# Kernel tuning notes

Measured on AMD Instinct MI355X. Metric: run time of the kernel, lower is better.

The kernel has to match this reference:

```python
import jax, jax.numpy as jnp
import numpy as np

B = 16
N = [20000, 5000, 1250, 313, 79]          # node counts per pooling level (fine -> coarse)
E = [120000, 30000, 7500, 1878, 474]      # ~6 edges per node (triangle mesh)
FILTERS = [3, 32, 32, 64, 64, 64]
K = 6
Z = 64
COND = 2
N_LAYERS = 4


def setup_inputs():
    ks = iter(jax.random.split(jax.random.key(0), 64))
    inp = {}
    inp["x"] = jax.random.normal(next(ks), (B * N[0], FILTERS[0]), jnp.float32)
    inp["label"] = jax.random.normal(next(ks), (B, COND), jnp.float32)
    for i in range(5):
        inp[f"edges{i}"] = jax.random.randint(next(ks), (2, E[i]), 0, N[i])
    for i in range(4):
        inp[f"ds_idx{i}"] = jax.random.randint(next(ks), (N[i + 1],), 0, N[i])
        inp[f"us_idx{i}"] = jax.random.randint(next(ks), (N[i], 3), 0, N[i + 1])
        inp[f"us_w{i}"] = jax.random.uniform(next(ks), (N[i], 3), jnp.float32)
    for i in range(4):
        inp[f"enc_w{i}"] = 0.1 * jax.random.normal(next(ks), (K, FILTERS[i], FILTERS[i + 1]), jnp.float32)
        inp[f"enc_b{i}"] = 0.1 * jax.random.normal(next(ks), (FILTERS[i + 1],), jnp.float32)
    for i in range(5):
        inp[f"dec_w{i}"] = 0.1 * jax.random.normal(next(ks), (K, FILTERS[-i - 1], FILTERS[-i - 2]), jnp.float32)
    for i in range(4):
        inp[f"dec_b{i}"] = 0.1 * jax.random.normal(next(ks), (FILTERS[-i - 2],), jnp.float32)
    lat_in = N[4] * FILTERS[-1]
    inp["enc_mu_w"] = 0.1 * jax.random.normal(next(ks), (lat_in, Z), jnp.float32)
    inp["enc_mu_b"] = jnp.zeros((Z,), jnp.float32)
    inp["enc_lv_w"] = 0.1 * jax.random.normal(next(ks), (lat_in, Z), jnp.float32)
    inp["enc_lv_b"] = jnp.zeros((Z,), jnp.float32)
    inp["dec_lin_w"] = 0.1 * jax.random.normal(next(ks), (Z + COND, lat_in), jnp.float32)
    inp["dec_lin_b"] = jnp.zeros((lat_in,), jnp.float32)
    return inp


def _sym_norm(edges, n):
    # ChebConv_Coma.norm: norm = D^-1/2[row] * w * D^-1/2[col], unit weights
    row, col = edges[0], edges[1]
    deg = jnp.zeros((n,), jnp.float32).at[row].add(1.0)
    dinv = jnp.where(deg > 0, deg ** -0.5, 0.0)
    return dinv[row] * dinv[col]


def _cheb(x, edges, norm, W, b):
    # Chebyshev recursion: Tx_0=x, Tx_1=L~x, Tx_k=2 L~ Tx_{k-1} - Tx_{k-2}
    src, tgt = edges[0], edges[1]

    def prop(h):  # h: [B, Nn, F] -> scatter-sum of norm-weighted source features
        return jnp.zeros_like(h).at[:, tgt].add(h[:, src] * norm[None, :, None])

    Tx0 = x
    out = jnp.einsum('bnf,fg->bng', Tx0, W[0])
    Tx1 = prop(x)
    out = out + jnp.einsum('bnf,fg->bng', Tx1, W[1])
    for k in range(2, W.shape[0]):
        Tx2 = 2.0 * prop(Tx1) - Tx0
        out = out + jnp.einsum('bnf,fg->bng', Tx2, W[k])
        Tx0, Tx1 = Tx1, Tx2
    return out if b is None else out + b


def _forward(x, label, us_ws, enc_ws, enc_bs, dec_ws, dec_bs,
             enc_mu_w, enc_mu_b, enc_lv_w, enc_lv_b, dec_lin_w, dec_lin_b,
             edges, norms, ds_idx, us_idx):
    h = x.reshape(B, N[0], FILTERS[0])
    # encoder
    for i in range(N_LAYERS):
        h = jax.nn.relu(_cheb(h, edges[i], norms[i], enc_ws[i], enc_bs[i]))
        h = h[:, ds_idx[i]]  # binary downsample matrix == row gather
    h = h.reshape(B, N[4] * FILTERS[-1])
    mu = h @ enc_mu_w + enc_mu_b
    logvar = h @ enc_lv_w + enc_lv_b
    # reparameterize (fixed eps for determinism)
    eps = jax.random.normal(jax.random.key(42), mu.shape, mu.dtype)
    z = mu + eps * jnp.exp(0.5 * logvar)
    # decoder
    h = jnp.concatenate([z, label], axis=1)
    h = jax.nn.relu(h @ dec_lin_w + dec_lin_b).reshape(B, N[4], FILTERS[-1])
    for i in range(N_LAYERS):
        lvl = N_LAYERS - 1 - i
        # barycentric upsample: 3 nonzeros per output row
        h = jnp.einsum('rk,brkf->brf', us_ws[lvl], h[:, us_idx[lvl]])
        h = jax.nn.relu(_cheb(h, edges[lvl], norms[lvl], dec_ws[i], dec_bs[i]))
    # faithful quirk of the original: final conv uses A_edge_index[-1] (coarsest graph edges)
    h = _cheb(h, edges[-1], norms[-1], dec_ws[4], None)
    return h.reshape(-1, FILTERS[0]), mu, logvar


def reference(x, label,
              edges0, edges1, edges2, edges3, edges4,
              ds_idx0, ds_idx1, ds_idx2, ds_idx3,
              us_idx0, us_idx1, us_idx2, us_idx3,
              us_w0, us_w1, us_w2, us_w3,
              enc_w0, enc_w1, enc_w2, enc_w3,
              enc_b0, enc_b1, enc_b2, enc_b3,
              dec_w0, dec_w1, dec_w2, dec_w3, dec_w4,
              dec_b0, dec_b1, dec_b2, dec_b3,
              enc_mu_w, enc_mu_b, enc_lv_w, enc_lv_b, dec_lin_w, dec_lin_b):
    edges = [edges0, edges1, edges2, edges3, edges4]
    norms = [_sym_norm(edges[i], N[i]) for i in range(5)]
    return _forward(x, label,
                    [us_w0, us_w1, us_w2, us_w3],
                    [enc_w0, enc_w1, enc_w2, enc_w3],
                    [enc_b0, enc_b1, enc_b2, enc_b3],
                    [dec_w0, dec_w1, dec_w2, dec_w3, dec_w4],
                    [dec_b0, dec_b1, dec_b2, dec_b3],
                    enc_mu_w, enc_mu_b, enc_lv_w, enc_lv_b, dec_lin_w, dec_lin_b,
                    edges, norms,
                    [ds_idx0, ds_idx1, ds_idx2, ds_idx3],
                    [us_idx0, us_idx1, us_idx2, us_idx3])
```

## Files before the change

### kernel.cpp

```cpp
#include <hip/hip_runtime.h>
#include <cstdint>
#include <cstddef>

#define WG 256
#define NB 16



__global__ void k_zero_i(int* __restrict__ p, int n) {
  int i = blockIdx.x * WG + threadIdx.x;
  if (i < n) p[i] = 0;
}

__global__ void k_hist(const int* __restrict__ edges, int E,
                       int* __restrict__ dsrc, int* __restrict__ dtgt) {
  int e = blockIdx.x * WG + threadIdx.x;
  if (e >= E) return;
  atomicAdd(&dsrc[edges[e]], 1);
  atomicAdd(&dtgt[edges[E + e]], 1);
}

__global__ void k_scan(const int* __restrict__ deg, int N,
                       int* __restrict__ rowptr, int* __restrict__ cursor) {
  __shared__ int s[WG];
  int t = threadIdx.x;
  int chunk = (N + WG - 1) / WG;
  int a = t * chunk;
  int b = min(N, a + chunk);
  int sum = 0;
  for (int i = a; i < b; i++) sum += deg[i];
  s[t] = sum;
  __syncthreads();
  for (int off = 1; off < WG; off <<= 1) {
    int v = (t >= off) ? s[t - off] : 0;
    __syncthreads();
    s[t] += v;
    __syncthreads();
  }
  int run = (t == 0) ? 0 : s[t - 1];
  for (int i = a; i < b; i++) {
    rowptr[i] = run;
    cursor[i] = run;
    run += deg[i];
  }
  if (t == 0) rowptr[N] = s[WG - 1];
}

__global__ void k_fill(const int* __restrict__ edges, int E,
                       const int* __restrict__ dsrc, int* __restrict__ cursor,
                       int* __restrict__ csrc, float* __restrict__ csw) {
  int e = blockIdx.x * WG + threadIdx.x;
  if (e >= E) return;
  int s = edges[e], t = edges[E + e];
  float da = (float)dsrc[s], db = (float)dsrc[t];
  float wa = (da > 0.f) ? (1.0f / sqrtf(da)) : 0.f;
  float wb = (db > 0.f) ? (1.0f / sqrtf(db)) : 0.f;
  int pos = atomicAdd(&cursor[t], 1);
  csrc[pos] = s;
  csw[pos] = wa * wb;
}

__global__ void k_tr_x(const float* __restrict__ x, float* __restrict__ out) {
  int i = blockIdx.x * WG + threadIdx.x;
  if (i >= NB * 20000 * 3) return;
  int f = i % 3;
  int b = (i / 3) % NB;
  int n = i / 48;
  out[i] = x[((size_t)b * 20000 + n) * 3 + f];
}


static __device__ __forceinline__ float erfinv_f(float x) {
  float w = -log1pf(-x * x);
  float p;
  if (w < 5.0f) {
    w -= 2.5f;
    p = 2.81022636e-08f;
    p = fmaf(p, w, 3.43273939e-07f);
    p = fmaf(p, w, -3.5233877e-06f);
    p = fmaf(p, w, -4.39150654e-06f);
    p = fmaf(p, w, 0.00021858087f);
    p = fmaf(p, w, -0.00125372503f);
    p = fmaf(p, w, -0.00417768164f);
    p = fmaf(p, w, 0.246640727f);
    p = fmaf(p, w, 1.50140941f);
  } else {
    w = sqrtf(w) - 3.0f;
    p = -0.000200214257f;
    p = fmaf(p, w, 0.000100950558f);
    p = fmaf(p, w, 0.00134934322f);
    p = fmaf(p, w, -0.00367342844f);
    p = fmaf(p, w, 0.00573950773f);
    p = fmaf(p, w, -0.0076224613f);
    p = fmaf(p, w, 0.00943887047f);
    p = fmaf(p, w, 1.00167406f);
    p = fmaf(p, w, 2.83297682f);
  }
  return p * x;
}

static __device__ __forceinline__ float bits_to_normal(unsigned b) {
  float f = __uint_as_float((b >> 9) | 0x3f800000u) - 1.0f;
  const float lo = -0.99999994f;
  float u = f * (1.0f - lo) + lo;
  u = fmaxf(u, lo);
  return 1.41421356f * erfinv_f(u);
}

__global__ void k_eps(float* __restrict__ eps) {
  int i = blockIdx.x * WG + threadIdx.x;
  if (i >= 1024) return;
  unsigned x0 = 0u, x1 = (unsigned)i;
  unsigned ks[3] = {0u, 42u, 0u ^ 42u ^ 0x1BD11BDAu};
  x0 += ks[0];
  x1 += ks[1];
  const int R[2][4] = {{13, 15, 26, 6}, {17, 29, 16, 24}};
#pragma unroll
  for (int it = 0; it < 5; it++) {
#pragma unroll
    for (int j = 0; j < 4; j++) {
      x0 += x1;
      int r = R[it & 1][j];
      x1 = (x1 << r) | (x1 >> (32 - r));
      x1 ^= x0;
    }
    x0 += ks[(it + 1) % 3];
    x1 += ks[(it + 2) % 3] + (unsigned)(it + 1);
  }
  eps[i] = bits_to_normal(x0 ^ x1);
}


template <int F>
__global__ __launch_bounds__(WG) void k_propw(const float* __restrict__ in,
                                              float* __restrict__ out,
                                              const float* __restrict__ sub, float scale,
                                              const int* __restrict__ rowptr,
                                              const int* __restrict__ csrc,
                                              const float* __restrict__ csw, int N) {
  constexpr int C4 = F / 16;
  int node = blockIdx.x * 4 + (threadIdx.x >> 6);
  if (node >= N) return;
  int lane = threadIdx.x & 63;
  const float4* in4 = (const float4*)in;
  float4 acc[C4];
#pragma unroll
  for (int u = 0; u < C4; u++) acc[u] = make_float4(0.f, 0.f, 0.f, 0.f);
  int beg = rowptr[node], end = rowptr[node + 1];
  int j = beg;
  for (; j + 1 < end; j += 2) {
    int s0 = __builtin_amdgcn_readfirstlane(csrc[j]);
    int s1 = __builtin_amdgcn_readfirstlane(csrc[j + 1]);
    float w0 = __int_as_float(__builtin_amdgcn_readfirstlane(__float_as_int(csw[j])));
    float w1 = __int_as_float(__builtin_amdgcn_readfirstlane(__float_as_int(csw[j + 1])));
    const float4* r0 = in4 + (size_t)s0 * (4 * F) + lane;
    const float4* r1 = in4 + (size_t)s1 * (4 * F) + lane;
#pragma unroll
    for (int u = 0; u < C4; u++) {
      float4 v0 = r0[u * 64];
      float4 v1 = r1[u * 64];
      acc[u].x = fmaf(w0, v0.x, acc[u].x); acc[u].y = fmaf(w0, v0.y, acc[u].y);
      acc[u].z = fmaf(w0, v0.z, acc[u].z); acc[u].w = fmaf(w0, v0.w, acc[u].w);
      acc[u].x = fmaf(w1, v1.x, acc[u].x); acc[u].y = fmaf(w1, v1.y, acc[u].y);
      acc[u].z = fmaf(w1, v1.z, acc[u].z); acc[u].w = fmaf(w1, v1.w, acc[u].w);
    }
  }
  if (j < end) {
    int s0 = __builtin_amdgcn_readfirstlane(csrc[j]);
    float w0 = __int_as_float(__builtin_amdgcn_readfirstlane(__float_as_int(csw[j])));
    const float4* r0 = in4 + (size_t)s0 * (4 * F) + lane;
#pragma unroll
    for (int u = 0; u < C4; u++) {
      float4 v0 = r0[u * 64];
      acc[u].x = fmaf(w0, v0.x, acc[u].x); acc[u].y = fmaf(w0, v0.y, acc[u].y);
      acc[u].z = fmaf(w0, v0.z, acc[u].z); acc[u].w = fmaf(w0, v0.w, acc[u].w);
    }
  }
  float4* o4 = (float4*)out + (size_t)node * (4 * F) + lane;
  if (sub) {
    const float4* s4 = (const float4*)sub + (size_t)node * (4 * F) + lane;
#pragma unroll
    for (int u = 0; u < C4; u++) {
      float4 sv = s4[u * 64];
      float4 r;
      r.x = fmaf(scale, acc[u].x, -sv.x); r.y = fmaf(scale, acc[u].y, -sv.y);
      r.z = fmaf(scale, acc[u].z, -sv.z); r.w = fmaf(scale, acc[u].w, -sv.w);
      o4[u * 64] = r;
    }
  } else {
#pragma unroll
    for (int u = 0; u < C4; u++) {
      float4 r;
      r.x = scale * acc[u].x; r.y = scale * acc[u].y;
      r.z = scale * acc[u].z; r.w = scale * acc[u].w;
      o4[u * 64] = r;
    }
  }
}

__global__ __launch_bounds__(WG) void k_propw3(const float* __restrict__ in,
                                               float* __restrict__ out,
                                               const float* __restrict__ sub, float scale,
                                               const int* __restrict__ rowptr,
                                               const int* __restrict__ csrc,
                                               const float* __restrict__ csw, int N) {
  int node = blockIdx.x * 4 + (threadIdx.x >> 6);
  if (node >= N) return;
  int lane = threadIdx.x & 63;
  if (lane >= 48) return;
  float acc = 0.f;
  int beg = rowptr[node], end = rowptr[node + 1];
  for (int j = beg; j < end; j++) {
    int s = __builtin_amdgcn_readfirstlane(csrc[j]);
    float w = __int_as_float(__builtin_amdgcn_readfirstlane(__float_as_int(csw[j])));
    acc = fmaf(w, in[(size_t)s * 48 + lane], acc);
  }
  float r = scale * acc;
  if (sub) r -= sub[(size_t)node * 48 + lane];
  out[(size_t)node * 48 + lane] = r;
}

struct Ptr3 {
  const float* p[3];
};

template <int F, int G>
__global__ __launch_bounds__(WG) void k_gemm3(Ptr3 txs, const float* __restrict__ W,
                                              const float* __restrict__ bias,
                                              float* __restrict__ out, int rows,
                                              int accum, int relu) {
  constexpr int CG = G / 4;
  constexpr int RPB = WG / CG;
  __shared__ float sW[3 * F * G];
  for (int i = threadIdx.x; i < 3 * F * G; i += WG) sW[i] = W[i];
  __syncthreads();
  int cg = threadIdx.x % CG;
  int r = threadIdx.x / CG;
  int row = blockIdx.x * RPB + r;
  if (row >= rows) return;
  float* o = out + (size_t)row * G + cg * 4;
  float4 a;
  if (accum) {
    a = *(const float4*)o;
  } else if (bias) {
    a = *(const float4*)(bias + cg * 4);
  } else {
    a = make_float4(0.f, 0.f, 0.f, 0.f);
  }
#pragma unroll
  for (int kk = 0; kk < 3; kk++) {
    const float* t = txs.p[kk] + (size_t)row * F;
    const float* w = sW + kk * F * G + cg * 4;
    if constexpr (F == 3) {
      float x0 = t[0], x1 = t[1], x2 = t[2];
      float4 w0 = *(const float4*)(w + 0 * G);
      float4 w1 = *(const float4*)(w + 1 * G);
      float4 w2 = *(const float4*)(w + 2 * G);
      a.x = fmaf(x0, w0.x, a.x); a.y = fmaf(x0, w0.y, a.y); a.z = fmaf(x0, w0.z, a.z); a.w = fmaf(x0, w0.w, a.w);
      a.x = fmaf(x1, w1.x, a.x); a.y = fmaf(x1, w1.y, a.y); a.z = fmaf(x1, w1.z, a.z); a.w = fmaf(x1, w1.w, a.w);
      a.x = fmaf(x2, w2.x, a.x); a.y = fmaf(x2, w2.y, a.y); a.z = fmaf(x2, w2.z, a.z); a.w = fmaf(x2, w2.w, a.w);
    } else {
#pragma unroll
      for (int f = 0; f < F; f += 4) {
        float4 xv = *(const float4*)(t + f);
        float4 w0 = *(const float4*)(w + (f + 0) * G);
        float4 w1 = *(const float4*)(w + (f + 1) * G);
        float4 w2 = *(const float4*)(w + (f + 2) * G);
        float4 w3 = *(const float4*)(w + (f + 3) * G);
        a.x = fmaf(xv.x, w0.x, a.x); a.y = fmaf(xv.x, w0.y, a.y); a.z = fmaf(xv.x, w0.z, a.z); a.w = fmaf(xv.x, w0.w, a.w);
        a.x = fmaf(xv.y, w1.x, a.x); a.y = fmaf(xv.y, w1.y, a.y); a.z = fmaf(xv.y, w1.z, a.z); a.w = fmaf(xv.y, w1.w, a.w);
        a.x = fmaf(xv.z, w2.x, a.x); a.y = fmaf(xv.z, w2.y, a.y); a.z = fmaf(xv.z, w2.z, a.z); a.w = fmaf(xv.z, w2.w, a.w);
        a.x = fmaf(xv.w, w3.x, a.x); a.y = fmaf(xv.w, w3.y, a.y); a.z = fmaf(xv.w, w3.z, a.z); a.w = fmaf(xv.w, w3.w, a.w);
      }
    }
  }
  if (relu) {
    a.x = fmaxf(a.x, 0.f); a.y = fmaxf(a.y, 0.f);
    a.z = fmaxf(a.z, 0.f); a.w = fmaxf(a.w, 0.f);
  }
  *(float4*)o = a;
}

__global__ __launch_bounds__(WG) void k_final_short(const float* __restrict__ in,
                                                    const float* __restrict__ W,
                                                    float* __restrict__ out) {
  __shared__ float sW[96];
  if (threadIdx.x < 96)
    sW[threadIdx.x] = W[threadIdx.x] - W[192 + threadIdx.x] + W[384 + threadIdx.x];
  __syncthreads();
  int tid = blockIdx.x * WG + threadIdx.x;
  if (tid >= NB * 20000) return;
  int b = tid / 20000, n = tid % 20000;
  const float* t = in + ((size_t)n * 16 + b) * 32;
  float a0 = 0.f, a1 = 0.f, a2 = 0.f;
#pragma unroll
  for (int f = 0; f < 32; f += 4) {
    float4 v = *(const float4*)(t + f);
    a0 = fmaf(v.x, sW[(f + 0) * 3 + 0], a0); a1 = fmaf(v.x, sW[(f + 0) * 3 + 1], a1); a2 = fmaf(v.x, sW[(f + 0) * 3 + 2], a2);
    a0 = fmaf(v.y, sW[(f + 1) * 3 + 0], a0); a1 = fmaf(v.y, sW[(f + 1) * 3 + 1], a1); a2 = fmaf(v.y, sW[(f + 1) * 3 + 2], a2);
    a0 = fmaf(v.z, sW[(f + 2) * 3 + 0], a0); a1 = fmaf(v.z, sW[(f + 2) * 3 + 1], a1); a2 = fmaf(v.z, sW[(f + 2) * 3 + 2], a2);
    a0 = fmaf(v.w, sW[(f + 3) * 3 + 0], a0); a1 = fmaf(v.w, sW[(f + 3) * 3 + 1], a1); a2 = fmaf(v.w, sW[(f + 3) * 3 + 2], a2);
  }
  float* o = out + (size_t)tid * 3;
  o[0] = a0; o[1] = a1; o[2] = a2;
}

__global__ __launch_bounds__(256) void k_final_fix(const float* __restrict__ in,
                                                   const float* __restrict__ W,
                                                   const int* __restrict__ rowptr,
                                                   const int* __restrict__ csrc,
                                                   const float* __restrict__ csw,
                                                   float* __restrict__ out) {
  __shared__ float B0[79 * 32], B1[79 * 32], B2[79 * 32];
  __shared__ float sacc[79 * 3];
  __shared__ float sW[576];
  int b = blockIdx.x, t = threadIdx.x;
  for (int i = t; i < 576; i += 256) sW[i] = W[i];
  for (int i = t; i < 2528; i += 256) {
    int r = i >> 5, f = i & 31;
    B0[i] = in[((size_t)r * 16 + b) * 32 + f];
  }
  __syncthreads();
  for (int i = t; i < 237; i += 256) {
    int r = i / 3, g = i % 3;
    float a = 0.f;
    for (int f = 0; f < 32; f++) a = fmaf(B0[r * 32 + f], sW[f * 3 + g], a);
    sacc[i] = a;
  }
  for (int i = t; i < 2528; i += 256) {
    int r = i >> 5, f = i & 31;
    float a = 0.f;
    for (int j = rowptr[r]; j < rowptr[r + 1]; j++) a = fmaf(csw[j], B0[csrc[j] * 32 + f], a);
    B1[i] = a;
  }
  __syncthreads();
  for (int i = t; i < 237; i += 256) {
    int r = i / 3, g = i % 3;
    float a = sacc[i];
    for (int f = 0; f < 32; f++) a = fmaf(B1[r * 32 + f], sW[96 + f * 3 + g], a);
    sacc[i] = a;
  }
  for (int i = t; i < 2528; i += 256) {
    int r = i >> 5, f = i & 31;
    float a = 0.f;
    for (int j = rowptr[r]; j < rowptr[r + 1]; j++) a = fmaf(csw[j], B1[csrc[j] * 32 + f], a);
    B2[i] = 2.f * a - B0[i];
  }
  __syncthreads();
  for (int i = t; i < 237; i += 256) {
    int r = i / 3, g = i % 3;
    float a = sacc[i];
    for (int f = 0; f < 32; f++) a = fmaf(B2[r * 32 + f], sW[192 + f * 3 + g], a);
    sacc[i] = a;
  }
  __syncthreads();
  for (int i = t; i < 2528; i += 256) {
    int r = i >> 5, f = i & 31;
    float a = 0.f;
    for (int j = rowptr[r]; j < rowptr[r + 1]; j++) a = fmaf(csw[j], B2[csrc[j] * 32 + f], a);
    B0[i] = 2.f * a - B1[i];
  }
  __syncthreads();
  for (int i = t; i < 237; i += 256) {
    int r = i / 3, g = i % 3;
    float a = sacc[i];
    for (int f = 0; f < 32; f++) a = fmaf(B0[r * 32 + f], sW[288 + f * 3 + g], a);
    sacc[i] = a;
  }
  __syncthreads();
  for (int i = t; i < 2528; i += 256) {
    int r = i >> 5, f = i & 31;
    float a = 0.f;
    for (int j = rowptr[r]; j < rowptr[r + 1]; j++) a = fmaf(csw[j], B0[csrc[j] * 32 + f], a);
    B1[i] = 2.f * a - B2[i];
  }
  __syncthreads();
  for (int i = t; i < 237; i += 256) {
    int r = i / 3, g = i % 3;
    float a = sacc[i];
    for (int f = 0; f < 32; f++) a = fmaf(B1[r * 32 + f], sW[384 + f * 3 + g], a);
    sacc[i] = a;
  }
  __syncthreads();
  for (int i = t; i < 2528; i += 256) {
    int r = i >> 5, f = i & 31;
    float a = 0.f;
    for (int j = rowptr[r]; j < rowptr[r + 1]; j++) a = fmaf(csw[j], B1[csrc[j] * 32 + f], a);
    B2[i] = 2.f * a - B0[i];
  }
  __syncthreads();
  for (int i = t; i < 237; i += 256) {
    int r = i / 3, g = i % 3;
    float a = sacc[i];
    for (int f = 0; f < 32; f++) a = fmaf(B2[r * 32 + f], sW[480 + f * 3 + g], a);
    out[((size_t)b * 20000 + r) * 3 + g] = a;
  }
}

template <int F>
__global__ __launch_bounds__(WG) void k_ds(const float* __restrict__ in,
                                           float* __restrict__ out,
                                           const int* __restrict__ idx, int Nout) {
  int i = blockIdx.x * WG + threadIdx.x;
  int total = Nout * NB * F;
  if (i >= total) return;
  int pos = i % (NB * F);
  int j = i / (NB * F);
  float v = in[(size_t)idx[j] * NB * F + pos];
  out[i] = fmaxf(v, 0.f);
}

template <int F>
__global__ __launch_bounds__(WG) void k_us(const float* __restrict__ in,
                                           float* __restrict__ out,
                                           const int* __restrict__ uidx,
                                           const float* __restrict__ uw, int Nf) {
  int i = blockIdx.x * WG + threadIdx.x;
  int total = Nf * NB * F;
  if (i >= total) return;
  int pos = i % (NB * F);
  int r = i / (NB * F);
  float acc = 0.f;
#pragma unroll
  for (int k = 0; k < 3; k++) {
    float v = in[(size_t)uidx[r * 3 + k] * NB * F + pos];
    acc = fmaf(uw[r * 3 + k], fmaxf(v, 0.f), acc);
  }
  out[i] = acc;
}


__global__ __launch_bounds__(64) void k_latent(const float* __restrict__ h,
                                               const float* __restrict__ muW,
                                               const float* __restrict__ muB,
                                               const float* __restrict__ lvW,
                                               const float* __restrict__ lvB,
                                               const float* __restrict__ eps,
                                               const float* __restrict__ label,
                                               float* __restrict__ mu_out,
                                               float* __restrict__ lv_out,
                                               float* __restrict__ hcat) {
  int b = blockIdx.x / 64;
  int g = blockIdx.x % 64;
  int l = threadIdx.x;
  float am = 0.f, al = 0.f;
  for (int i = l; i < 5056; i += 64) {
    int n = i >> 6, f = i & 63;
    float hv = h[(size_t)(n * 16 + b) * 64 + f];
    am = fmaf(hv, muW[(size_t)i * 64 + g], am);
    al = fmaf(hv, lvW[(size_t)i * 64 + g], al);
  }
  for (int off = 32; off > 0; off >>= 1) {
    am += __shfl_down(am, off, 64);
    al += __shfl_down(al, off, 64);
  }
  if (l == 0) {
    am += muB[g];
    al += lvB[g];
    mu_out[b * 64 + g] = am;
    lv_out[b * 64 + g] = al;
    hcat[b * 66 + g] = fmaf(eps[b * 64 + g], expf(0.5f * al), am);
    if (g < 2) hcat[b * 66 + 64 + g] = label[b * 2 + g];
  }
}

__global__ __launch_bounds__(WG) void k_declin(const float* __restrict__ hcat,
                                               const float* __restrict__ W,
                                               const float* __restrict__ bias,
                                               float* __restrict__ out) {
  int idx = blockIdx.x * WG + threadIdx.x;
  if (idx >= NB * 5056) return;
  int b = idx / 5056, j = idx % 5056;
  int n = j >> 6, f = j & 63;
  float acc = bias[j];
  const float* hc = hcat + b * 66;
#pragma unroll
  for (int i = 0; i < 66; i++) acc = fmaf(hc[i], W[(size_t)i * 5056 + j], acc);
  out[(size_t)(n * 16 + b) * 64 + f] = fmaxf(acc, 0.f);
}


static inline dim3 grid1(long n) { return dim3((unsigned)((n + WG - 1) / WG)); }

template <int F, int G>
static void run_cheb(float* in, float* out, float* A, float* B,
                     const float* W, const float* bias, int N, int relu_last,
                     const int* rowptr, const int* csrc, const float* csw,
                     hipStream_t st) {
  int rows = NB * N;
  constexpr int RPB = WG / (G / 4);
  dim3 gG((unsigned)((rows + RPB - 1) / RPB));
  dim3 gP((unsigned)((N + 3) / 4));
  if constexpr (F == 3) {
    k_propw3<<<gP, WG, 0, st>>>(in, A, nullptr, 1.f, rowptr, csrc, csw, N);
    k_propw3<<<gP, WG, 0, st>>>(A, B, in, 2.f, rowptr, csrc, csw, N);
    Ptr3 p1{{in, A, B}};
    k_gemm3<F, G><<<gG, WG, 0, st>>>(p1, W, bias, out, rows, 0, 0);
    k_propw3<<<gP, WG, 0, st>>>(B, in, A, 2.f, rowptr, csrc, csw, N);
    k_propw3<<<gP, WG, 0, st>>>(in, A, B, 2.f, rowptr, csrc, csw, N);
    k_propw3<<<gP, WG, 0, st>>>(A, B, in, 2.f, rowptr, csrc, csw, N);
    Ptr3 p2{{in, A, B}};
    k_gemm3<F, G><<<gG, WG, 0, st>>>(p2, W + 3 * F * G, nullptr, out, rows, 1, relu_last);
  } else {
    k_propw<F><<<gP, WG, 0, st>>>(in, A, nullptr, 1.f, rowptr, csrc, csw, N);
    k_propw<F><<<gP, WG, 0, st>>>(A, B, in, 2.f, rowptr, csrc, csw, N);
    Ptr3 p1{{in, A, B}};
    k_gemm3<F, G><<<gG, WG, 0, st>>>(p1, W, bias, out, rows, 0, 0);
    k_propw<F><<<gP, WG, 0, st>>>(B, in, A, 2.f, rowptr, csrc, csw, N);
    k_propw<F><<<gP, WG, 0, st>>>(in, A, B, 2.f, rowptr, csrc, csw, N);
    k_propw<F><<<gP, WG, 0, st>>>(A, B, in, 2.f, rowptr, csrc, csw, N);
    Ptr3 p2{{in, A, B}};
    k_gemm3<F, G><<<gG, WG, 0, st>>>(p2, W + 3 * F * G, nullptr, out, rows, 1, relu_last);
  }
}

extern "C" void kernel_launch(void* const* d_in, const int* in_sizes, int n_in,
                              void* d_out, int out_size, void* d_ws, size_t ws_size,
                              hipStream_t stream) {
  static const int NN[5] = {20000, 5000, 1250, 313, 79};
  static const int EE[5] = {120000, 30000, 7500, 1878, 474};
  static const int NCSR[5] = {20000, 5000, 1250, 313, 20000};

  const float* x = (const float*)d_in[0];
  const float* label = (const float*)d_in[1];
  const int* edges[5];
  for (int l = 0; l < 5; l++) edges[l] = (const int*)d_in[2 + l];
  const int* ds_idx[4];
  const int* us_idx[4];
  const float* us_w[4];
  for (int i = 0; i < 4; i++) {
    ds_idx[i] = (const int*)d_in[7 + 3 * i];
    us_idx[i] = (const int*)d_in[8 + 3 * i];
    us_w[i] = (const float*)d_in[9 + 3 * i];
  }
  const float* enc_w[4];
  const float* enc_b[4];
  for (int i = 0; i < 4; i++) {
    enc_w[i] = (const float*)d_in[19 + 2 * i];
    enc_b[i] = (const float*)d_in[20 + 2 * i];
  }
  const float* dec_w[5];
  for (int i = 0; i < 5; i++) dec_w[i] = (const float*)d_in[27 + i];
  const float* dec_b[4];
  for (int i = 0; i < 4; i++) dec_b[i] = (const float*)d_in[32 + i];
  const float* mu_w = (const float*)d_in[36];
  const float* mu_b = (const float*)d_in[37];
  const float* lv_w = (const float*)d_in[38];
  const float* lv_b = (const float*)d_in[39];
  const float* dl_w = (const float*)d_in[40];
  const float* dl_b = (const float*)d_in[41];

  float* wsf = (float*)d_ws;
  size_t off = 0;
  auto carve = [&](size_t n) -> float* {
    float* p = wsf + off;
    off += (n + 63) & ~(size_t)63;
    return p;
  };
  const size_t SLOT = 10240000;
  float* s0 = carve(SLOT);
  float* s1 = carve(SLOT);
  float* s2 = carve(SLOT);
  float* s3 = carve(SLOT);
  float* sxl = carve(960000);
  int* deg_all = (int*)carve(26642 + 46563);
  int* deg_src_all = deg_all;
  int* deg_tgt_all = deg_all + 26642;
  int* rowptr_all = (int*)carve(46568);
  int* cursor_all = (int*)carve(46563);
  int* csrc_all = (int*)carve(159852);
  float* csw_all = carve(159852);
  float* eps = carve(1024);
  float* hcat = carve(1056);

  int NOFF[5], COFF[5], ROFF[5], EOFF[5];
  {
    int na = 0, ca = 0, ra = 0, ea = 0;
    for (int l = 0; l < 5; l++) {
      NOFF[l] = na; na += NN[l];
      COFF[l] = ca; ca += NCSR[l];
      ROFF[l] = ra; ra += NCSR[l] + 1;
      EOFF[l] = ea; ea += EE[l];
    }
  }

  k_zero_i<<<grid1(26642 + 46563), WG, 0, stream>>>(deg_all, 26642 + 46563);
  for (int l = 0; l < 5; l++)
    k_hist<<<grid1(EE[l]), WG, 0, stream>>>(edges[l], EE[l], deg_src_all + NOFF[l],
                                            deg_tgt_all + COFF[l]);
  for (int l = 0; l < 5; l++)
    k_scan<<<1, WG, 0, stream>>>(deg_tgt_all + COFF[l], NCSR[l], rowptr_all + ROFF[l],
                                 cursor_all + COFF[l]);
  for (int l = 0; l < 5; l++)
    k_fill<<<grid1(EE[l]), WG, 0, stream>>>(edges[l], EE[l], deg_src_all + NOFF[l],
                                            cursor_all + COFF[l], csrc_all + EOFF[l],
                                            csw_all + EOFF[l]);
  k_eps<<<4, WG, 0, stream>>>(eps);
  k_tr_x<<<grid1(960000), WG, 0, stream>>>(x, sxl);

  auto RP = [&](int l) { return rowptr_all + ROFF[l]; };
  auto CS = [&](int l) { return csrc_all + EOFF[l]; };
  auto CW = [&](int l) { return csw_all + EOFF[l]; };

  float* mu_out = (float*)d_out + 960000;
  float* lv_out = (float*)d_out + 961024;

  run_cheb<3, 32>(sxl, s0, s2, s3, enc_w[0], enc_b[0], 20000, 0, RP(0), CS(0), CW(0), stream);
  k_ds<32><<<grid1((long)5000 * NB * 32), WG, 0, stream>>>(s0, s1, ds_idx[0], 5000);
  run_cheb<32, 32>(s1, s0, s2, s3, enc_w[1], enc_b[1], 5000, 0, RP(1), CS(1), CW(1), stream);
  k_ds<32><<<grid1((long)1250 * NB * 32), WG, 0, stream>>>(s0, s1, ds_idx[1], 1250);
  run_cheb<32, 64>(s1, s0, s2, s3, enc_w[2], enc_b[2], 1250, 0, RP(2), CS(2), CW(2), stream);
  k_ds<64><<<grid1((long)313 * NB * 64), WG, 0, stream>>>(s0, s1, ds_idx[2], 313);
  run_cheb<64, 64>(s1, s0, s2, s3, enc_w[3], enc_b[3], 313, 0, RP(3), CS(3), CW(3), stream);
  k_ds<64><<<grid1((long)79 * NB * 64), WG, 0, stream>>>(s0, s1, ds_idx[3], 79);

  k_latent<<<1024, 64, 0, stream>>>(s1, mu_w, mu_b, lv_w, lv_b, eps, label, mu_out, lv_out, hcat);
  k_declin<<<grid1(NB * 5056), WG, 0, stream>>>(hcat, dl_w, dl_b, s0);

  k_us<64><<<grid1((long)313 * NB * 64), WG, 0, stream>>>(s0, s1, us_idx[3], us_w[3], 313);
  run_cheb<64, 64>(s1, s0, s2, s3, dec_w[0], dec_b[0], 313, 0, RP(3), CS(3), CW(3), stream);
  k_us<64><<<grid1((long)1250 * NB * 64), WG, 0, stream>>>(s0, s1, us_idx[2], us_w[2], 1250);
  run_cheb<64, 64>(s1, s0, s2, s3, dec_w[1], dec_b[1], 1250, 0, RP(2), CS(2), CW(2), stream);
  k_us<64><<<grid1((long)5000 * NB * 64), WG, 0, stream>>>(s0, s1, us_idx[1], us_w[1], 5000);
  run_cheb<64, 32>(s1, s0, s2, s3, dec_w[2], dec_b[2], 5000, 0, RP(1), CS(1), CW(1), stream);
  k_us<32><<<grid1((long)20000 * NB * 32), WG, 0, stream>>>(s0, s1, us_idx[0], us_w[0], 20000);
  run_cheb<32, 32>(s1, s0, s2, s3, dec_w[3], dec_b[3], 20000, 1, RP(0), CS(0), CW(0), stream);

  k_final_short<<<grid1(NB * 20000), WG, 0, stream>>>(s0, dec_w[4], (float*)d_out);
  k_final_fix<<<16, 256, 0, stream>>>(s0, dec_w[4], RP(4), CS(4), CW(4), (float*)d_out);
}
```

Before: 1.358 ms.

## Fuse downsample gather into Chebyshev GEMM and tile four rows per thread

Encoder Chebyshev layers now compute their output GEMM only for the pooled nodes, gathering source rows via the downsample index and applying ReLU in the GEMM epilogue, which removes the separate k_ds kernels and avoids computing discarded rows. The GEMM kernel is also register-tiled so each thread computes four consecutive rows, reusing the shared-memory weight loads across rows. This raises register use per thread and relies on the four rows of a tile mapping to contiguous source rows.

```diff
diff --git a/kernel.cpp b/kernel.cpp
--- a/kernel.cpp
+++ b/kernel.cpp
@@ -228,57 +228,87 @@
 __global__ __launch_bounds__(WG) void k_gemm3(Ptr3 txs, const float* __restrict__ W,
                                               const float* __restrict__ bias,
                                               float* __restrict__ out, int rows,
+                                              const int* __restrict__ idx,
                                               int accum, int relu) {
   constexpr int CG = G / 4;
-  constexpr int RPB = WG / CG;
+  constexpr int RT = WG / CG;
+  constexpr int RPB = RT * 4;
   __shared__ float sW[3 * F * G];
   for (int i = threadIdx.x; i < 3 * F * G; i += WG) sW[i] = W[i];
   __syncthreads();
   int cg = threadIdx.x % CG;
-  int r = threadIdx.x / CG;
-  int row = blockIdx.x * RPB + r;
-  if (row >= rows) return;
-  float* o = out + (size_t)row * G + cg * 4;
-  float4 a;
+  int rt = threadIdx.x / CG;
+  int row0 = blockIdx.x * RPB + rt * 4;
+  if (row0 >= rows) return;
+  size_t src0;
+  if (idx) {
+    int node = row0 >> 4, b = row0 & 15;
+    src0 = (size_t)idx[node] * 16 + b;
+  } else {
+    src0 = (size_t)row0;
+  }
+  float* o = out + (size_t)row0 * G + cg * 4;
+  float4 acc[4];
   if (accum) {
-    a = *(const float4*)o;
+#pragma unroll
+    for (int r = 0; r < 4; r++) acc[r] = *(const float4*)(o + (size_t)r * G);
   } else if (bias) {
-    a = *(const float4*)(bias + cg * 4);
+    float4 bv = *(const float4*)(bias + cg * 4);
+#pragma unroll
+    for (int r = 0; r < 4; r++) acc[r] = bv;
   } else {
-    a = make_float4(0.f, 0.f, 0.f, 0.f);
+#pragma unroll
+    for (int r = 0; r < 4; r++) acc[r] = make_float4(0.f, 0.f, 0.f, 0.f);
   }
 #pragma unroll
   for (int kk = 0; kk < 3; kk++) {
-    const float* t = txs.p[kk] + (size_t)row * F;
+    const float* tb = txs.p[kk] + src0 * F;
     const float* w = sW + kk * F * G + cg * 4;
     if constexpr (F == 3) {
-      float x0 = t[0], x1 = t[1], x2 = t[2];
       float4 w0 = *(const float4*)(w + 0 * G);
       float4 w1 = *(const float4*)(w + 1 * G);
       float4 w2 = *(const float4*)(w + 2 * G);
-      a.x = fmaf(x0, w0.x, a.x); a.y = fmaf(x0, w0.y, a.y); a.z = fmaf(x0, w0.z, a.z); a.w = fmaf(x0, w0.w, a.w);
-      a.x = fmaf(x1, w1.x, a.x); a.y = fmaf(x1, w1.y, a.y); a.z = fmaf(x1, w1.z, a.z); a.w = fmaf(x1, w1.w, a.w);
-      a.x = fmaf(x2, w2.x, a.x); a.y = fmaf(x2, w2.y, a.y); a.z = fmaf(x2, w2.z, a.z); a.w = fmaf(x2, w2.w, a.w);
+#pragma unroll
+      for (int r = 0; r < 4; r++) {
+        float x0 = tb[r * 3 + 0], x1 = tb[r * 3 + 1], x2 = tb[r * 3 + 2];
+        acc[r].x = fmaf(x0, w0.x, acc[r].x); acc[r].y = fmaf(x0, w0.y, acc[r].y);
+        acc[r].z = fmaf(x0, w0.z, acc[r].z); acc[r].w = fmaf(x0, w0.w, acc[r].w);
+        acc[r].x = fmaf(x1, w1.x, acc[r].x); acc[r].y = fmaf(x1, w1.y, acc[r].y);
+        acc[r].z = fmaf(x1, w1.z, acc[r].z); acc[r].w = fmaf(x1, w1.w, acc[r].w);
+        acc[r].x = fmaf(x2, w2.x, acc[r].x); acc[r].y = fmaf(x2, w2.y, acc[r].y);
+        acc[r].z = fmaf(x2, w2.z, acc[r].z); acc[r].w = fmaf(x2, w2.w, acc[r].w);
+      }
     } else {
 #pragma unroll
-      for (int f = 0; f < F; f += 4) {
-        float4 xv = *(const float4*)(t + f);
-        float4 w0 = *(const float4*)(w + (f + 0) * G);
-        float4 w1 = *(const float4*)(w + (f + 1) * G);
-        float4 w2 = *(const float4*)(w + (f + 2) * G);
-        float4 w3 = *(const float4*)(w + (f + 3) * G);
-        a.x = fmaf(xv.x, w0.x, a.x); a.y = fmaf(xv.x, w0.y, a.y); a.z = fmaf(xv.x, w0.z, a.z); a.w = fmaf(xv.x, w0.w, a.w);
-        a.x = fmaf(xv.y, w1.x, a.x); a.y = fmaf(xv.y, w1.y, a.y); a.z = fmaf(xv.y, w1.z, a.z); a.w = fmaf(xv.y, w1.w, a.w);
-        a.x = fmaf(xv.z, w2.x, a.x); a.y = fmaf(xv.z, w2.y, a.y); a.z = fmaf(xv.z, w2.z, a.z); a.w = fmaf(xv.z, w2.w, a.w);
-        a.x = fmaf(xv.w, w3.x, a.x); a.y = fmaf(xv.w, w3.y, a.y); a.z = fmaf(xv.w, w3.z, a.z); a.w = fmaf(xv.w, w3.w, a.w);
+      for (int fg = 0; fg < F / 4; fg++) {
+        float4 w0 = *(const float4*)(w + (4 * fg + 0) * G);
+        float4 w1 = *(const float4*)(w + (4 * fg + 1) * G);
+        float4 w2 = *(const float4*)(w + (4 * fg + 2) * G);
+        float4 w3 = *(const float4*)(w + (4 * fg + 3) * G);
+#pragma unroll
+        for (int r = 0; r < 4; r++) {
+          float4 xv = *(const float4*)(tb + (size_t)r * F + 4 * fg);
+          acc[r].x = fmaf(xv.x, w0.x, acc[r].x); acc[r].y = fmaf(xv.x, w0.y, acc[r].y);
+          acc[r].z = fmaf(xv.x, w0.z, acc[r].z); acc[r].w = fmaf(xv.x, w0.w, acc[r].w);
+          acc[r].x = fmaf(xv.y, w1.x, acc[r].x); acc[r].y = fmaf(xv.y, w1.y, acc[r].y);
+          acc[r].z = fmaf(xv.y, w1.z, acc[r].z); acc[r].w = fmaf(xv.y, w1.w, acc[r].w);
+          acc[r].x = fmaf(xv.z, w2.x, acc[r].x); acc[r].y = fmaf(xv.z, w2.y, acc[r].y);
+          acc[r].z = fmaf(xv.z, w2.z, acc[r].z); acc[r].w = fmaf(xv.z, w2.w, acc[r].w);
+          acc[r].x = fmaf(xv.w, w3.x, acc[r].x); acc[r].y = fmaf(xv.w, w3.y, acc[r].y);
+          acc[r].z = fmaf(xv.w, w3.z, acc[r].z); acc[r].w = fmaf(xv.w, w3.w, acc[r].w);
+        }
       }
     }
   }
   if (relu) {
-    a.x = fmaxf(a.x, 0.f); a.y = fmaxf(a.y, 0.f);
-    a.z = fmaxf(a.z, 0.f); a.w = fmaxf(a.w, 0.f);
-  }
-  *(float4*)o = a;
+#pragma unroll
+    for (int r = 0; r < 4; r++) {
+      acc[r].x = fmaxf(acc[r].x, 0.f); acc[r].y = fmaxf(acc[r].y, 0.f);
+      acc[r].z = fmaxf(acc[r].z, 0.f); acc[r].w = fmaxf(acc[r].w, 0.f);
+    }
+  }
+#pragma unroll
+  for (int r = 0; r < 4; r++) *(float4*)(o + (size_t)r * G) = acc[r];
 }
 
 __global__ __launch_bounds__(WG) void k_final_short(const float* __restrict__ in,
@@ -395,19 +425,6 @@
     for (int f = 0; f < 32; f++) a = fmaf(B2[r * 32 + f], sW[480 + f * 3 + g], a);
     out[((size_t)b * 20000 + r) * 3 + g] = a;
   }
-}
-
-template <int F>
-__global__ __launch_bounds__(WG) void k_ds(const float* __restrict__ in,
-                                           float* __restrict__ out,
-                                           const int* __restrict__ idx, int Nout) {
-  int i = blockIdx.x * WG + threadIdx.x;
-  int total = Nout * NB * F;
-  if (i >= total) return;
-  int pos = i % (NB * F);
-  int j = i / (NB * F);
-  float v = in[(size_t)idx[j] * NB * F + pos];
-  out[i] = fmaxf(v, 0.f);
 }
 
 template <int F>
@@ -484,33 +501,35 @@
 
 template <int F, int G>
 static void run_cheb(float* in, float* out, float* A, float* B,
-                     const float* W, const float* bias, int N, int relu_last,
+                     const float* W, const float* bias, int N, int Nout,
+                     const int* ds_idx, int relu_last,
                      const int* rowptr, const int* csrc, const float* csw,
                      hipStream_t st) {
-  int rows = NB * N;
-  constexpr int RPB = WG / (G / 4);
-  dim3 gG((unsigned)((rows + RPB - 1) / RPB));
+  int orows = NB * Nout;
+  constexpr int RPB = (WG / (G / 4)) * 4;
+  dim3 gG((unsigned)((orows + RPB - 1) / RPB));
   dim3 gP((unsigned)((N + 3) / 4));
+  int relu2 = ds_idx ? 1 : relu_last;
   if constexpr (F == 3) {
     k_propw3<<<gP, WG, 0, st>>>(in, A, nullptr, 1.f, rowptr, csrc, csw, N);
     k_propw3<<<gP, WG, 0, st>>>(A, B, in, 2.f, rowptr, csrc, csw, N);
     Ptr3 p1{{in, A, B}};
-    k_gemm3<F, G><<<gG, WG, 0, st>>>(p1, W, bias, out, rows, 0, 0);
+    k_gemm3<F, G><<<gG, WG, 0, st>>>(p1, W, bias, out, orows, ds_idx, 0, 0);
     k_propw3<<<gP, WG, 0, st>>>(B, in, A, 2.f, rowptr, csrc, csw, N);
     k_propw3<<<gP, WG, 0, st>>>(in, A, B, 2.f, rowptr, csrc, csw, N);
     k_propw3<<<gP, WG, 0, st>>>(A, B, in, 2.f, rowptr, csrc, csw, N);
     Ptr3 p2{{in, A, B}};
-    k_gemm3<F, G><<<gG, WG, 0, st>>>(p2, W + 3 * F * G, nullptr, out, rows, 1, relu_last);
+    k_gemm3<F, G><<<gG, WG, 0, st>>>(p2, W + 3 * F * G, nullptr, out, orows, ds_idx, 1, relu2);
   } else {
     k_propw<F><<<gP, WG, 0, st>>>(in, A, nullptr, 1.f, rowptr, csrc, csw, N);
     k_propw<F><<<gP, WG, 0, st>>>(A, B, in, 2.f, rowptr, csrc, csw, N);
     Ptr3 p1{{in, A, B}};
-    k_gemm3<F, G><<<gG, WG, 0, st>>>(p1, W, bias, out, rows, 0, 0);
+    k_gemm3<F, G><<<gG, WG, 0, st>>>(p1, W, bias, out, orows, ds_idx, 0, 0);
     k_propw<F><<<gP, WG, 0, st>>>(B, in, A, 2.f, rowptr, csrc, csw, N);
     k_propw<F><<<gP, WG, 0, st>>>(in, A, B, 2.f, rowptr, csrc, csw, N);
     k_propw<F><<<gP, WG, 0, st>>>(A, B, in, 2.f, rowptr, csrc, csw, N);
     Ptr3 p2{{in, A, B}};
-    k_gemm3<F, G><<<gG, WG, 0, st>>>(p2, W + 3 * F * G, nullptr, out, rows, 1, relu_last);
+    k_gemm3<F, G><<<gG, WG, 0, st>>>(p2, W + 3 * F * G, nullptr, out, orows, ds_idx, 1, relu2);
   }
 }
 
@@ -605,26 +624,30 @@
   float* mu_out = (float*)d_out + 960000;
   float* lv_out = (float*)d_out + 961024;
 
-  run_cheb<3, 32>(sxl, s0, s2, s3, enc_w[0], enc_b[0], 20000, 0, RP(0), CS(0), CW(0), stream);
-  k_ds<32><<<grid1((long)5000 * NB * 32), WG, 0, stream>>>(s0, s1, ds_idx[0], 5000);
-  run_cheb<32, 32>(s1, s0, s2, s3, enc_w[1], enc_b[1], 5000, 0, RP(1), CS(1), CW(1), stream);
-  k_ds<32><<<grid1((long)1250 * NB * 32), WG, 0, stream>>>(s0, s1, ds_idx[1], 1250);
-  run_cheb<32, 64>(s1, s0, s2, s3, enc_w[2], enc_b[2], 1250, 0, RP(2), CS(2), CW(2), stream);
-  k_ds<64><<<grid1((long)313 * NB * 64), WG, 0, stream>>>(s0, s1, ds_idx[2], 313);
-  run_cheb<64, 64>(s1, s0, s2, s3, enc_w[3], enc_b[3], 313, 0, RP(3), CS(3), CW(3), stream);
-  k_ds<64><<<grid1((long)79 * NB * 64), WG, 0, stream>>>(s0, s1, ds_idx[3], 79);
-
-  k_latent<<<1024, 64, 0, stream>>>(s1, mu_w, mu_b, lv_w, lv_b, eps, label, mu_out, lv_out, hcat);
+  run_cheb<3, 32>(sxl, s1, s2, s3, enc_w[0], enc_b[0], 20000, 5000, ds_idx[0], 0,
+                  RP(0), CS(0), CW(0), stream);
+  run_cheb<32, 32>(s1, s0, s2, s3, enc_w[1], enc_b[1], 5000, 1250, ds_idx[1], 0,
+                   RP(1), CS(1), CW(1), stream);
+  run_cheb<32, 64>(s0, s1, s2, s3, enc_w[2], enc_b[2], 1250, 313, ds_idx[2], 0,
+                   RP(2), CS(2), CW(2), stream);
+  run_cheb<64, 64>(s1, s0, s2, s3, enc_w[3], enc_b[3], 313, 79, ds_idx[3], 0,
+                   RP(3), CS(3), CW(3), stream);
+
+  k_latent<<<1024, 64, 0, stream>>>(s0, mu_w, mu_b, lv_w, lv_b, eps, label, mu_out, lv_out, hcat);
   k_declin<<<grid1(NB * 5056), WG, 0, stream>>>(hcat, dl_w, dl_b, s0);
 
   k_us<64><<<grid1((long)313 * NB * 64), WG, 0, stream>>>(s0, s1, us_idx[3], us_w[3], 313);
-  run_cheb<64, 64>(s1, s0, s2, s3, dec_w[0], dec_b[0], 313, 0, RP(3), CS(3), CW(3), stream);
+  run_cheb<64, 64>(s1, s0, s2, s3, dec_w[0], dec_b[0], 313, 313, nullptr, 0,
+                   RP(3), CS(3), CW(3), stream);
   k_us<64><<<grid1((long)1250 * NB * 64), WG, 0, stream>>>(s0, s1, us_idx[2], us_w[2], 1250);
-  run_cheb<64, 64>(s1, s0, s2, s3, dec_w[1], dec_b[1], 1250, 0, RP(2), CS(2), CW(2), stream);
+  run_cheb<64, 64>(s1, s0, s2, s3, dec_w[1], dec_b[1], 1250, 1250, nullptr, 0,
+                   RP(2), CS(2), CW(2), stream);
   k_us<64><<<grid1((long)5000 * NB * 64), WG, 0, stream>>>(s0, s1, us_idx[1], us_w[1], 5000);
-  run_cheb<64, 32>(s1, s0, s2, s3, dec_w[2], dec_b[2], 5000, 0, RP(1), CS(1), CW(1), stream);
+  run_cheb<64, 32>(s1, s0, s2, s3, dec_w[2], dec_b[2], 5000, 5000, nullptr, 0,
+                   RP(1), CS(1), CW(1), stream);
   k_us<32><<<grid1((long)20000 * NB * 32), WG, 0, stream>>>(s0, s1, us_idx[0], us_w[0], 20000);
-  run_cheb<32, 32>(s1, s0, s2, s3, dec_w[3], dec_b[3], 20000, 1, RP(0), CS(0), CW(0), stream);
+  run_cheb<32, 32>(s1, s0, s2, s3, dec_w[3], dec_b[3], 20000, 20000, nullptr, 1,
+                   RP(0), CS(0), CW(0), stream);
 
   k_final_short<<<grid1(NB * 20000), WG, 0, stream>>>(s0, dec_w[4], (float*)d_out);
   k_final_fix<<<16, 256, 0, stream>>>(s0, dec_w[4], RP(4), CS(4), CW(4), (float*)d_out);
```

Result: faster. 1.325 ms (-2.4%).
